# Optimization experiments

Measured on AMD Instinct MI355X. Metric: run time of the kernel, lower is better.

The kernel has to match this reference:

```python
import jax, jax.numpy as jnp
import numpy as np

B, SEQ, OBS, HID = 32, 50, 1024, 256


def setup_inputs() -> dict:
    key = jax.random.key(0)
    k = jax.random.split(key, 6)
    y = jax.random.normal(k[0], (B, SEQ, OBS), jnp.float32)
    logdet = jax.random.normal(k[1], (B * SEQ,), jnp.float32)
    U_param = jax.random.normal(k[2], (HID, HID), jnp.float32)
    V_param = jax.random.normal(k[3], (HID, HID), jnp.float32)
    # torch init sets alpha to small constant 0.001; use small positive values
    alpha = jax.random.uniform(k[4], (HID,), jnp.float32) * 0.01
    # C initialized as orthonormal-ish (svd-projected xavier); scale to unit-norm columns
    C = jax.random.normal(k[5], (OBS, HID), jnp.float32) / np.sqrt(OBS).astype(np.float32)
    return {"y": y, "logdet": logdet, "U_param": U_param, "V_param": V_param,
            "alpha": alpha, "C": C}


def _unitary(Up):
    """Product of dim Householder reflections, combined by pairwise doubling."""
    dim = Up.shape[0]
    Un = Up / jnp.linalg.norm(Up, axis=1, keepdims=True)
    # UH[i] = I - 2 u_i u_i^T   -> (dim, dim, dim)
    M = jnp.eye(dim, dtype=Up.dtype)[None] - 2.0 * Un[:, :, None] * Un[:, None, :]
    n = dim
    while n > 1:  # log2(dim) fixed steps (multi_matmul_power_of_two)
        n //= 2
        M = jnp.matmul(M[:n], M[n:])
    return M[0]


def reference(y, logdet, U_param, V_param, alpha, C):
    U = _unitary(U_param)
    V = _unitary(V_param)
    S = 1.0 - jnp.clip(jnp.abs(alpha), 0.0, 1.0)          # SV()
    A = U @ (S[None, :] * V.T)                             # build_A

    s = y.shape[1]
    obs, hid = C.shape

    # build_O_A: O = [C; C A; C A^2; ...] via scan (matrix-power recurrence)
    def step(T, _):
        return T @ A, T
    _, Os = jax.lax.scan(step, C, None, length=s)          # (s, obs, hid)
    O = Os.reshape(s * obs, hid)

    Y = y.reshape(y.shape[0], -1)                          # (b, s*obs)

    # torch.gels(Y.t(), O): least-squares solve, x0 detached
    x0 = jax.lax.stop_gradient(
        jnp.linalg.lstsq(jax.lax.stop_gradient(O), jax.lax.stop_gradient(Y.T))[0]
    )                                                      # (hid, b)

    Yhat = O @ x0                                          # (s*obs, b)
    w = Y.T - Yhat
    M = jnp.float32(obs)                                   # prod(xflat.shape[1:])
    loss = 0.5 * jnp.mean(w ** 2) + jnp.mean((logdet / M) ** 2)
    return loss


if __name__ == "__main__":
    print(reference(**setup_inputs()))
```

## Files before the change

kernel.cpp:

```cpp
#include <hip/hip_runtime.h>

#define HID 256
#define OBS 1024
#define SEQ 50
#define BATCH 32
#define SO (SEQ*OBS)

struct DevWS {
  float ub[2][HID][HID];
  float C2[2][HID][HID];
  float ZT[2][HID][HID];
  float U[HID][HID];
  float V[HID][HID];
  float A[HID][HID];
  float A2[HID][HID];
  float A4[HID][HID];
  float A8[HID][HID];
  float A16[HID][HID];
  float A32[HID][HID];
  float Cg[HID][HID];
  float G2[HID][HID];
  float Grun[HID][HID];
  float T[HID][HID];
  float T2[HID][HID];
  float G18[HID][HID];
  float G32b[HID][HID];
  float Gfin[HID][HID];
  float Zt[SEQ][HID*BATCH];
  float Rb[2][25][HID*BATCH];
  float psum[1025];
  float s1b[32];
};
__device__ DevWS g;

__device__ __forceinline__ float* sel(int c){
  switch(c){
    case 0:  return &g.ub[0][0][0];
    case 1:  return &g.ub[1][0][0];
    case 4:  return &g.C2[0][0][0];
    case 5:  return &g.C2[1][0][0];
    case 6:  return &g.ZT[0][0][0];
    case 7:  return &g.ZT[1][0][0];
    case 8:  return &g.U[0][0];
    case 9:  return &g.V[0][0];
    case 10: return &g.A[0][0];
    case 11: return &g.A2[0][0];
    case 12: return &g.A4[0][0];
    case 13: return &g.A8[0][0];
    case 14: return &g.A16[0][0];
    case 15: return &g.A32[0][0];
    case 16: return &g.Cg[0][0];
    case 17: return &g.G2[0][0];
    case 18: return &g.Grun[0][0];
    case 19: return &g.T[0][0];
    case 20: return &g.T2[0][0];
    case 21: return &g.G18[0][0];
    case 22: return &g.G32b[0][0];
    case 23: return &g.Gfin[0][0];
    case 24: return &g.Zt[0][0];
    case 25: return &g.Rb[0][0][0];
    default: return &g.Rb[1][0][0];
  }
}

__device__ __forceinline__ int bitrev8(int x){
  x = ((x & 0x55) << 1) | ((x >> 1) & 0x55);
  x = ((x & 0x33) << 2) | ((x >> 2) & 0x33);
  x = ((x & 0x0F) << 4) | ((x >> 4) & 0x0F);
  return x;
}

__global__ __launch_bounds__(256) void k_prep(const float* __restrict__ y,
                                              const float* __restrict__ logdet,
                                              const float* __restrict__ Up,
                                              const float* __restrict__ Vp,
                                              const float* __restrict__ Cm){
  __shared__ float As[16][36];
  __shared__ float Bs[16][36];
  __shared__ float red[256];
  const int bx = blockIdx.x;
  const int t = threadIdx.x;
  if(bx < 512){
    int mat = bx >> 8, j = bx & 255;
    int src = bitrev8(j);
    const float* P = mat ? Vp : Up;
    float x = P[src*HID + t];
    red[t] = x*x; __syncthreads();
    for(int s=128; s>0; s>>=1){ if(t<s) red[t]+=red[t+s]; __syncthreads(); }
    g.ub[mat][j][t] = x * rsqrtf(red[0]);
    return;
  }
  if(bx < 1536){
    int bi = bx - 512;
    const float4* y4 = reinterpret_cast<const float4*>(y);
    const int n4 = (BATCH*SO)/4;
    float s = 0.f;
    for(int i = bi*256 + t; i < n4; i += 1024*256){
      float4 v = y4[i];
      s += v.x*v.x + v.y*v.y + v.z*v.z + v.w*v.w;
    }
    red[t] = s; __syncthreads();
    for(int st=128; st>0; st>>=1){ if(t<st) red[t]+=red[t+st]; __syncthreads(); }
    if(t==0) g.psum[bi] = red[0];
    return;
  }
  if(bx == 1536){
    float s = 0.f;
    for(int i = t; i < BATCH*SEQ; i += 256){ float v = logdet[i]; s += v*v; }
    red[t] = s; __syncthreads();
    for(int st=128; st>0; st>>=1){ if(t<st) red[t]+=red[t+st]; __syncthreads(); }
    if(t==0) g.psum[1024] = red[0];
    return;
  }
  {
    int tile = bx - 1537;
    int tx = t & 15, ty = t >> 4;
    int m0 = (tile>>3)*32, n0 = (tile&7)*32;
    float acc[2][2] = {{0.f,0.f},{0.f,0.f}};
    for(int o0=0; o0<OBS; o0+=16){
      int r = t>>4, cp = (t&15)*2;
      float2 a = *reinterpret_cast<const float2*>(&Cm[(o0+r)*HID + m0 + cp]);
      As[r][cp] = a.x; As[r][cp+1] = a.y;
      float2 b = *reinterpret_cast<const float2*>(&Cm[(o0+r)*HID + n0 + cp]);
      Bs[r][cp] = b.x; Bs[r][cp+1] = b.y;
      __syncthreads();
      #pragma unroll
      for(int kk=0; kk<16; kk++){
        float a0 = As[kk][ty*2], a1 = As[kk][ty*2+1];
        float b0 = Bs[kk][tx*2], b1 = Bs[kk][tx*2+1];
        acc[0][0]+=a0*b0; acc[0][1]+=a0*b1; acc[1][0]+=a1*b0; acc[1][1]+=a1*b1;
      }
      __syncthreads();
    }
    #pragma unroll
    for(int i2=0;i2<2;i2++)
    #pragma unroll
    for(int j2=0;j2<2;j2++)
      g.Cg[m0+ty*2+i2][n0+tx*2+j2] = acc[i2][j2];
  }
}

__global__ __launch_bounds__(1024) void k_CtY(const float* __restrict__ y,
                                              const float* __restrict__ C){
  const int tt = blockIdx.x;
  __shared__ float ys[256][36];
  const int h = threadIdx.x >> 2, bq = threadIdx.x & 3;
  float acc[8] = {0,0,0,0,0,0,0,0};
  for(int ot=0; ot<4; ot++){
    for(int e=threadIdx.x; e<32*256; e+=1024){
      int b = e>>8, o = e&255;
      ys[o][b] = y[b*SO + tt*OBS + ot*256 + o];
    }
    __syncthreads();
    for(int o=0; o<256; o++){
      float cv = C[(ot*256+o)*HID + h];
      float4 v0 = *reinterpret_cast<const float4*>(&ys[o][bq*8]);
      float4 v1 = *reinterpret_cast<const float4*>(&ys[o][bq*8+4]);
      acc[0]+=cv*v0.x; acc[1]+=cv*v0.y; acc[2]+=cv*v0.z; acc[3]+=cv*v0.w;
      acc[4]+=cv*v1.x; acc[5]+=cv*v1.y; acc[6]+=cv*v1.z; acc[7]+=cv*v1.w;
    }
    __syncthreads();
  }
  #pragma unroll
  for(int j=0;j<8;j++) g.Zt[tt][h*32 + bq*8 + j] = acc[j];
}

__global__ __launch_bounds__(1024) void k_wy(){
  const int m = blockIdx.x;
  const int t = threadIdx.x;
  __shared__ float c2s[32][256];
  __shared__ float ws[32][256];
  for(int p=0; p<8; p++){
    const int k0 = p*32;
    for(int e=t; e<32*256; e+=1024){
      int k = e>>8, i = e&255;
      c2s[k][i] = (i < k0+k) ? g.C2[m][k0+k][i] : 0.f;
    }
    __syncthreads();
    {
      int d = t & 255, kg = t>>8;
      float acc[8] = {0,0,0,0,0,0,0,0};
      for(int i=0; i<k0; i++){
        float zv = g.ZT[m][i][d];
        #pragma unroll
        for(int kk=0; kk<8; kk++) acc[kk] += zv * c2s[kg*8+kk][i];
      }
      #pragma unroll
      for(int kk=0; kk<8; kk++) ws[kg*8+kk][d] = acc[kk];
    }
    __syncthreads();
    if(t < 256){
      const int d = t;
      float zreg[32];
      #pragma unroll
      for(int j=0;j<32;j++) zreg[j] = 0.f;
      #pragma unroll
      for(int k=0; k<32; k++){
        float a0=0.f,a1=0.f,a2=0.f,a3=0.f;
        #pragma unroll
        for(int j=0;j<32;j+=4){
          a0 += zreg[j]  *c2s[k][k0+j];
          a1 += zreg[j+1]*c2s[k][k0+j+1];
          a2 += zreg[j+2]*c2s[k][k0+j+2];
          a3 += zreg[j+3]*c2s[k][k0+j+3];
        }
        float acc = (a0+a1)+(a2+a3);
        zreg[k] = 2.f*(g.ub[m][k0+k][d] - ws[k][d] - acc);
      }
      #pragma unroll
      for(int k=0; k<32; k++) g.ZT[m][k0+k][d] = zreg[k];
    }
    __syncthreads();
  }
}

#define F_TRANSA   1
#define F_NEGID    2
#define F_ACC      4
#define F_TRANSB   8
#define F_SCALECOL 16
#define F_RLEVEL   32

struct GD { int cA, cB, cC, cD, flags, npair; };
struct GArgs { GD d[3]; int pre[3]; int nd; };

__global__ __launch_bounds__(256) void k_gemmN(GArgs ga, const float* __restrict__ alpha){
  int blk = blockIdx.x;
  int di = 0;
  if(ga.nd > 1 && blk >= ga.pre[1]) di = 1;
  if(ga.nd > 2 && blk >= ga.pre[2]) di = 2;
  const GD d = ga.d[di];
  const int local = blk - ga.pre[di];
  const int t = threadIdx.x;
  __shared__ float As[16][36];
  __shared__ float Bs[16][36];
  const int tx = t & 15, ty = t >> 4;

  if(d.flags & F_RLEVEL){
    const float* P  = sel(d.cA);
    const float* In = sel(d.cB);
    float* Out = sel(d.cC);
    const int j = local >> 3, mt = local & 7;
    if(j >= d.npair){
      const float* src = In + (size_t)(2*j)*(HID*BATCH) + mt*1024;
      float* dst = Out + (size_t)j*(HID*BATCH) + mt*1024;
      *reinterpret_cast<float4*>(dst + t*4) = *reinterpret_cast<const float4*>(src + t*4);
      return;
    }
    const float* B1 = In + (size_t)(2*j+1)*(HID*BATCH);
    const float* D0 = In + (size_t)(2*j)*(HID*BATCH);
    float* C0 = Out + (size_t)j*(HID*BATCH);
    const int m0 = mt*32;
    float acc[2][2] = {{0.f,0.f},{0.f,0.f}};
    for(int k0=0; k0<HID; k0+=16){
      { int kk=t>>4, mm=(t&15)*2;
        float2 a = *reinterpret_cast<const float2*>(&P[(k0+kk)*HID + m0+mm]);
        As[kk][mm]=a.x; As[kk][mm+1]=a.y; }
      { int rb=t>>4, cb=(t&15)*2;
        float2 b = *reinterpret_cast<const float2*>(&B1[(k0+rb)*BATCH + cb]);
        Bs[rb][cb]=b.x; Bs[rb][cb+1]=b.y; }
      __syncthreads();
      #pragma unroll
      for(int kk=0; kk<16; kk++){
        float a0=As[kk][ty*2], a1=As[kk][ty*2+1];
        float b0=Bs[kk][tx*2], b1=Bs[kk][tx*2+1];
        acc[0][0]+=a0*b0; acc[0][1]+=a0*b1; acc[1][0]+=a1*b0; acc[1][1]+=a1*b1;
      }
      __syncthreads();
    }
    #pragma unroll
    for(int i2=0;i2<2;i2++)
    #pragma unroll
    for(int j2=0;j2<2;j2++){
      int r=m0+ty*2+i2, c=tx*2+j2;
      C0[r*BATCH+c] = D0[r*BATCH+c] + acc[i2][j2];
    }
    return;
  }

  const float* A = sel(d.cA);
  const float* B = sel(d.cB);
  float* Cp = sel(d.cC);
  const float* Dp = sel(d.cD);
  const int m0 = (local>>3)*32, n0 = (local&7)*32;
  float acc[2][2] = {{0.f,0.f},{0.f,0.f}};
  for(int k0=0; k0<HID; k0+=16){
    if(d.flags & F_TRANSA){
      int kk=t>>4, mm=(t&15)*2;
      float2 a = *reinterpret_cast<const float2*>(&A[(k0+kk)*HID + m0+mm]);
      As[kk][mm]=a.x; As[kk][mm+1]=a.y;
    } else {
      int r=t>>3, c=(t&7)*2;
      float2 a = *reinterpret_cast<const float2*>(&A[(m0+r)*HID + k0+c]);
      As[c][r]=a.x; As[c+1][r]=a.y;
    }
    if(d.flags & F_TRANSB){
      int cb=t>>3, rb=(t&7)*2;
      float2 v = *reinterpret_cast<const float2*>(&B[(n0+cb)*HID + k0+rb]);
      Bs[rb][cb]=v.x; Bs[rb+1][cb]=v.y;
    } else {
      int rb=t>>4, cb=(t&15)*2;
      float2 b = *reinterpret_cast<const float2*>(&B[(k0+rb)*HID + n0+cb]);
      Bs[rb][cb]=b.x; Bs[rb][cb+1]=b.y;
    }
    __syncthreads();
    #pragma unroll
    for(int kk=0; kk<16; kk++){
      float a0=As[kk][ty*2], a1=As[kk][ty*2+1];
      float b0=Bs[kk][tx*2], b1=Bs[kk][tx*2+1];
      acc[0][0]+=a0*b0; acc[0][1]+=a0*b1; acc[1][0]+=a1*b0; acc[1][1]+=a1*b1;
    }
    __syncthreads();
  }
  float sc0=1.f, sc1=1.f;
  if(d.flags & F_SCALECOL){
    sc0 = 1.0f - fminf(fabsf(alpha[n0+tx*2]),   1.0f);
    sc1 = 1.0f - fminf(fabsf(alpha[n0+tx*2+1]), 1.0f);
  }
  #pragma unroll
  for(int i2=0;i2<2;i2++)
  #pragma unroll
  for(int j2=0;j2<2;j2++){
    int r=m0+ty*2+i2, c=n0+tx*2+j2;
    float v = acc[i2][j2];
    if(d.flags & F_ACC) v += Dp[r*HID+c];
    if(d.flags & F_SCALECOL) v *= (j2 ? sc1 : sc0);
    if(d.flags & F_NEGID) v = (r==c ? 1.0f : 0.0f) - v;
    Cp[r*HID+c] = v;
  }
}

#define CG_ITERS 10
__global__ __launch_bounds__(1024) void k_cg(){
  const int tid = threadIdx.x;
  const int i = tid & 255;
  const int q = tid >> 8;
  const int lane = tid & 63;
  const int wv = tid >> 6;
  const int b0 = blockIdx.x * 4;
  __shared__ float p_s[256][4];
  __shared__ float partf[4][256][4];
  __shared__ float red1[16];
  __shared__ float s_rz[4], s_pap[4], s_rzn[4], s_be[4], s_s1[4];

  float gr[64];
  const float* Gf = &g.Gfin[0][0];
  #pragma unroll
  for(int j=0;j<64;j++) gr[j] = Gf[(64*q+j)*HID + i];
  const float dinv = 1.0f / Gf[i*(HID+1)];

  float rcur = g.Rb[1][0][i*BATCH + b0 + q];
  p_s[i][q] = rcur*dinv;
  if(tid<4) s_s1[tid]=0.f;
  __syncthreads();

  {
    float v = dinv*rcur*rcur;
    v+=__shfl_down(v,32);v+=__shfl_down(v,16);v+=__shfl_down(v,8);
    v+=__shfl_down(v,4);v+=__shfl_down(v,2);v+=__shfl_down(v,1);
    if(lane==0) red1[wv]=v;
    __syncthreads();
    if(tid<4) s_rz[tid]=red1[tid*4]+red1[tid*4+1]+red1[tid*4+2]+red1[tid*4+3];
    __syncthreads();
  }

  for(int it=0; it<CG_ITERS; it++){
    float pa0=0.f,pa1=0.f,pa2=0.f,pa3=0.f;
    #pragma unroll
    for(int j=0;j<64;j++){
      const float4 pv = *reinterpret_cast<const float4*>(&p_s[64*q+j][0]);
      const float gv = gr[j];
      pa0 = fmaf(gv,pv.x,pa0); pa1 = fmaf(gv,pv.y,pa1);
      pa2 = fmaf(gv,pv.z,pa2); pa3 = fmaf(gv,pv.w,pa3);
    }
    float4 w4; w4.x=pa0; w4.y=pa1; w4.z=pa2; w4.w=pa3;
    *reinterpret_cast<float4*>(&partf[q][i][0]) = w4;
    __syncthreads();
    const float ap = partf[0][i][q]+partf[1][i][q]+partf[2][i][q]+partf[3][i][q];
    const float pvl = p_s[i][q];
    {
      float v = pvl*ap;
      v+=__shfl_down(v,32);v+=__shfl_down(v,16);v+=__shfl_down(v,8);
      v+=__shfl_down(v,4);v+=__shfl_down(v,2);v+=__shfl_down(v,1);
      if(lane==0) red1[wv]=v;
      __syncthreads();
      if(tid<4) s_pap[tid]=red1[tid*4]+red1[tid*4+1]+red1[tid*4+2]+red1[tid*4+3];
      __syncthreads();
    }
    const float al = s_rz[q]/fmaxf(s_pap[q],1e-30f);
    rcur = rcur - al*ap;
    {
      float v = dinv*rcur*rcur;
      v+=__shfl_down(v,32);v+=__shfl_down(v,16);v+=__shfl_down(v,8);
      v+=__shfl_down(v,4);v+=__shfl_down(v,2);v+=__shfl_down(v,1);
      if(lane==0) red1[wv]=v;
      __syncthreads();
      if(tid<4) s_rzn[tid]=red1[tid*4]+red1[tid*4+1]+red1[tid*4+2]+red1[tid*4+3];
      __syncthreads();
    }
    if(tid<4){
      const float alb = s_rz[tid]/fmaxf(s_pap[tid],1e-30f);
      s_s1[tid] += alb*s_rz[tid];
      s_be[tid]  = s_rzn[tid]/fmaxf(s_rz[tid],1e-30f);
      s_rz[tid]  = s_rzn[tid];
    }
    __syncthreads();
    p_s[i][q] = dinv*rcur + s_be[q]*p_s[i][q];
    __syncthreads();
  }
  if(tid<4) g.s1b[b0+tid] = s_s1[tid];
}

__global__ __launch_bounds__(256) void k_fin(float* __restrict__ out){
  const int t = threadIdx.x;
  __shared__ float red[4];
  float s = g.psum[t] + g.psum[t+256] + g.psum[t+512] + g.psum[t+768];
  s += __shfl_down(s,32); s += __shfl_down(s,16); s += __shfl_down(s,8);
  s += __shfl_down(s,4);  s += __shfl_down(s,2);  s += __shfl_down(s,1);
  if((t&63)==0) red[t>>6]=s;
  __syncthreads();
  if(t==0){
    float sy2 = red[0]+red[1]+red[2]+red[3];
    float t1 = 0.f;
    for(int b=0;b<32;b++) t1 += g.s1b[b];
    float sld = g.psum[1024];
    float mw = (sy2 - t1) / (float)(SO*BATCH);
    out[0] = 0.5f*mw + sld / ((float)(BATCH*SEQ) * (float)OBS * (float)OBS);
  }
}

struct LB { GArgs ga; int total; };
static inline GD sq(int cA,int cB,int cC,int cD,int flags){ GD d; d.cA=cA;d.cB=cB;d.cC=cC;d.cD=cD;d.flags=flags;d.npair=0; return d; }
static inline GD rl(int cP,int cin,int cout,int npair){ GD d; d.cA=cP;d.cB=cin;d.cC=cout;d.cD=0;d.flags=F_RLEVEL;d.npair=npair; return d; }
static inline LB mk1(GD a,int ba){ LB l; l.ga.d[0]=a; l.ga.pre[0]=0; l.ga.pre[1]=ba; l.ga.pre[2]=ba; l.ga.nd=1; l.total=ba; return l; }
static inline LB mk2(GD a,int ba,GD b,int bb){ LB l; l.ga.d[0]=a; l.ga.d[1]=b; l.ga.pre[0]=0; l.ga.pre[1]=ba; l.ga.pre[2]=ba+bb; l.ga.nd=2; l.total=ba+bb; return l; }
static inline LB mk3(GD a,int ba,GD b,int bb,GD c,int bc){ LB l; l.ga.d[0]=a; l.ga.d[1]=b; l.ga.d[2]=c; l.ga.pre[0]=0; l.ga.pre[1]=ba; l.ga.pre[2]=ba+bb; l.ga.nd=3; l.total=ba+bb+bc; return l; }

extern "C" void kernel_launch(void* const* d_in, const int* in_sizes, int n_in,
                              void* d_out, int out_size, void* d_ws, size_t ws_size,
                              hipStream_t stream){
  const float* y      = (const float*)d_in[0];
  const float* logdet = (const float*)d_in[1];
  const float* Up     = (const float*)d_in[2];
  const float* Vp     = (const float*)d_in[3];
  const float* alpha  = (const float*)d_in[4];
  const float* Cm     = (const float*)d_in[5];
  float* out = (float*)d_out;

  k_prep<<<dim3(1601), dim3(256), 0, stream>>>(y, logdet, Up, Vp, Cm);
  k_CtY<<<dim3(SEQ), dim3(1024), 0, stream>>>(y, Cm);
  { LB l = mk2(sq(0,0,4,4,F_TRANSB),64, sq(1,1,5,5,F_TRANSB),64);
    k_gemmN<<<l.total,256,0,stream>>>(l.ga, alpha); }
  k_wy<<<dim3(2), dim3(1024), 0, stream>>>();
  { LB l = mk2(sq(6,0,8,8,F_TRANSA|F_NEGID),64, sq(7,1,9,9,F_TRANSA|F_NEGID),64);
    k_gemmN<<<l.total,256,0,stream>>>(l.ga, alpha); }
  { LB l = mk1(sq(8,9,10,10,F_TRANSB|F_SCALECOL),64);
    k_gemmN<<<l.total,256,0,stream>>>(l.ga, alpha); }
  { LB l = mk2(sq(10,10,11,0,0),64, sq(10,16,19,0,F_TRANSA),64);
    k_gemmN<<<l.total,256,0,stream>>>(l.ga, alpha); }
  { LB l = mk2(sq(19,10,17,16,F_ACC),64, rl(10,24,25,25),200);
    k_gemmN<<<l.total,256,0,stream>>>(l.ga, alpha); }
  { LB l = mk2(sq(11,11,12,0,0),64, sq(11,17,19,0,F_TRANSA),64);
    k_gemmN<<<l.total,256,0,stream>>>(l.ga, alpha); }
  { LB l = mk2(sq(19,11,18,17,F_ACC),64, rl(11,25,26,12),104);
    k_gemmN<<<l.total,256,0,stream>>>(l.ga, alpha); }
  { LB l = mk2(sq(12,12,13,0,0),64, sq(12,18,19,0,F_TRANSA),64);
    k_gemmN<<<l.total,256,0,stream>>>(l.ga, alpha); }
  { LB l = mk2(sq(19,12,18,18,F_ACC),64, rl(12,26,25,6),56);
    k_gemmN<<<l.total,256,0,stream>>>(l.ga, alpha); }
  { LB l = mk2(sq(13,13,14,0,0),64, sq(13,18,19,0,F_TRANSA),64);
    k_gemmN<<<l.total,256,0,stream>>>(l.ga, alpha); }
  { LB l = mk2(sq(19,13,18,18,F_ACC),64, rl(13,25,26,3),32);
    k_gemmN<<<l.total,256,0,stream>>>(l.ga, alpha); }
  { LB l = mk3(sq(14,14,15,0,0),64, sq(14,18,19,0,F_TRANSA),64, sq(14,17,20,0,F_TRANSA),64);
    k_gemmN<<<l.total,256,0,stream>>>(l.ga, alpha); }
  { LB l = mk3(sq(19,14,22,18,F_ACC),64, sq(20,14,21,18,F_ACC),64, rl(14,26,25,2),16);
    k_gemmN<<<l.total,256,0,stream>>>(l.ga, alpha); }
  { LB l = mk2(sq(15,21,19,0,F_TRANSA),64, rl(15,25,26,1),8);
    k_gemmN<<<l.total,256,0,stream>>>(l.ga, alpha); }
  { LB l = mk1(sq(19,15,23,22,F_ACC),64);
    k_gemmN<<<l.total,256,0,stream>>>(l.ga, alpha); }

  k_cg<<<dim3(8), dim3(1024), 0, stream>>>();
  k_fin<<<dim3(1), dim3(256), 0, stream>>>(out);
}
```

Before: 562.5 us.

## Fuse all stages into one persistent kernel with software grid barriers

Replaces the sequence of roughly twenty kernel launches with one persistent kernel of 256 blocks. The stages are separated by an atomic-counter grid barrier, which removes launch gaps and tail idle time. The serial single-block WY accumulation is replaced by a block-diagonal solve and a tree of merge steps. C^T Y is now split into more work units, and the CG solve is spread across the grid. The barrier depends on all 256 blocks being resident at the same time, and each stage now runs at low parallelism with the barrier cost paid between stages.

```diff
diff --git a/kernel.cpp b/kernel.cpp
--- a/kernel.cpp
+++ b/kernel.cpp
@@ -5,9 +5,18 @@
 #define SEQ 50
 #define BATCH 32
 #define SO (SEQ*OBS)
+#define NBLK 256
+#define NTHR 256
+
+#define F_TRANSA   1
+#define F_NEGID    2
+#define F_ACC      4
+#define F_TRANSB   8
+#define F_SCALECOL 16
 
 struct DevWS {
   float ub[2][HID][HID];
+  float Mm[2][HID][HID];
   float C2[2][HID][HID];
   float ZT[2][HID][HID];
   float U[HID][HID];
@@ -26,17 +35,40 @@
   float G18[HID][HID];
   float G32b[HID][HID];
   float Gfin[HID][HID];
-  float Zt[SEQ][HID*BATCH];
+  float Zt4[SEQ][4][HID*BATCH];
   float Rb[2][25][HID*BATCH];
-  float psum[1025];
-  float s1b[32];
+  float psum[NBLK+1];
+  float s1b[BATCH];
 };
 __device__ DevWS g;
+
+__device__ unsigned bar_in  = 0;
+__device__ unsigned bar_out = 0;
+
+__device__ __forceinline__ void gridbar(){
+  __threadfence();
+  __syncthreads();
+  if(threadIdx.x == 0){
+    atomicAdd(&bar_in, 1u);
+    while(atomicAdd(&bar_in, 0u) < (unsigned)NBLK){ __builtin_amdgcn_s_sleep(2); }
+    unsigned v = atomicAdd(&bar_out, 1u);
+    if(v == (unsigned)NBLK - 1u){
+      atomicExch(&bar_in, 0u);
+      atomicExch(&bar_out, 0u);
+    } else {
+      while(atomicAdd(&bar_out, 0u) != 0u){ __builtin_amdgcn_s_sleep(2); }
+    }
+  }
+  __syncthreads();
+  __threadfence();
+}
 
 __device__ __forceinline__ float* sel(int c){
   switch(c){
     case 0:  return &g.ub[0][0][0];
     case 1:  return &g.ub[1][0][0];
+    case 2:  return &g.Mm[0][0][0];
+    case 3:  return &g.Mm[1][0][0];
     case 4:  return &g.C2[0][0][0];
     case 5:  return &g.C2[1][0][0];
     case 6:  return &g.ZT[0][0][0];
@@ -57,7 +89,6 @@
     case 21: return &g.G18[0][0];
     case 22: return &g.G32b[0][0];
     case 23: return &g.Gfin[0][0];
-    case 24: return &g.Zt[0][0];
     case 25: return &g.Rb[0][0][0];
     default: return &g.Rb[1][0][0];
   }
@@ -70,371 +101,442 @@
   return x;
 }
 
-__global__ __launch_bounds__(256) void k_prep(const float* __restrict__ y,
-                                              const float* __restrict__ logdet,
-                                              const float* __restrict__ Up,
-                                              const float* __restrict__ Vp,
-                                              const float* __restrict__ Cm){
-  __shared__ float As[16][36];
-  __shared__ float Bs[16][36];
-  __shared__ float red[256];
-  const int bx = blockIdx.x;
+__device__ __forceinline__ float blkred(float v, float* sm){
+  v += __shfl_down(v,32); v += __shfl_down(v,16); v += __shfl_down(v,8);
+  v += __shfl_down(v,4);  v += __shfl_down(v,2);  v += __shfl_down(v,1);
   const int t = threadIdx.x;
-  if(bx < 512){
-    int mat = bx >> 8, j = bx & 255;
-    int src = bitrev8(j);
-    const float* P = mat ? Vp : Up;
-    float x = P[src*HID + t];
-    red[t] = x*x; __syncthreads();
-    for(int s=128; s>0; s>>=1){ if(t<s) red[t]+=red[t+s]; __syncthreads(); }
-    g.ub[mat][j][t] = x * rsqrtf(red[0]);
-    return;
-  }
-  if(bx < 1536){
-    int bi = bx - 512;
-    const float4* y4 = reinterpret_cast<const float4*>(y);
-    const int n4 = (BATCH*SO)/4;
-    float s = 0.f;
-    for(int i = bi*256 + t; i < n4; i += 1024*256){
-      float4 v = y4[i];
-      s += v.x*v.x + v.y*v.y + v.z*v.z + v.w*v.w;
-    }
-    red[t] = s; __syncthreads();
-    for(int st=128; st>0; st>>=1){ if(t<st) red[t]+=red[t+st]; __syncthreads(); }
-    if(t==0) g.psum[bi] = red[0];
-    return;
-  }
-  if(bx == 1536){
-    float s = 0.f;
-    for(int i = t; i < BATCH*SEQ; i += 256){ float v = logdet[i]; s += v*v; }
-    red[t] = s; __syncthreads();
-    for(int st=128; st>0; st>>=1){ if(t<st) red[t]+=red[t+st]; __syncthreads(); }
-    if(t==0) g.psum[1024] = red[0];
-    return;
-  }
-  {
-    int tile = bx - 1537;
-    int tx = t & 15, ty = t >> 4;
-    int m0 = (tile>>3)*32, n0 = (tile&7)*32;
-    float acc[2][2] = {{0.f,0.f},{0.f,0.f}};
-    for(int o0=0; o0<OBS; o0+=16){
-      int r = t>>4, cp = (t&15)*2;
-      float2 a = *reinterpret_cast<const float2*>(&Cm[(o0+r)*HID + m0 + cp]);
-      As[r][cp] = a.x; As[r][cp+1] = a.y;
-      float2 b = *reinterpret_cast<const float2*>(&Cm[(o0+r)*HID + n0 + cp]);
-      Bs[r][cp] = b.x; Bs[r][cp+1] = b.y;
-      __syncthreads();
-      #pragma unroll
-      for(int kk=0; kk<16; kk++){
-        float a0 = As[kk][ty*2], a1 = As[kk][ty*2+1];
-        float b0 = Bs[kk][tx*2], b1 = Bs[kk][tx*2+1];
-        acc[0][0]+=a0*b0; acc[0][1]+=a0*b1; acc[1][0]+=a1*b0; acc[1][1]+=a1*b1;
-      }
-      __syncthreads();
-    }
-    #pragma unroll
-    for(int i2=0;i2<2;i2++)
-    #pragma unroll
-    for(int j2=0;j2<2;j2++)
-      g.Cg[m0+ty*2+i2][n0+tx*2+j2] = acc[i2][j2];
-  }
-}
-
-__global__ __launch_bounds__(1024) void k_CtY(const float* __restrict__ y,
-                                              const float* __restrict__ C){
-  const int tt = blockIdx.x;
-  __shared__ float ys[256][36];
-  const int h = threadIdx.x >> 2, bq = threadIdx.x & 3;
-  float acc[8] = {0,0,0,0,0,0,0,0};
-  for(int ot=0; ot<4; ot++){
-    for(int e=threadIdx.x; e<32*256; e+=1024){
-      int b = e>>8, o = e&255;
-      ys[o][b] = y[b*SO + tt*OBS + ot*256 + o];
-    }
-    __syncthreads();
-    for(int o=0; o<256; o++){
-      float cv = C[(ot*256+o)*HID + h];
-      float4 v0 = *reinterpret_cast<const float4*>(&ys[o][bq*8]);
-      float4 v1 = *reinterpret_cast<const float4*>(&ys[o][bq*8+4]);
-      acc[0]+=cv*v0.x; acc[1]+=cv*v0.y; acc[2]+=cv*v0.z; acc[3]+=cv*v0.w;
-      acc[4]+=cv*v1.x; acc[5]+=cv*v1.y; acc[6]+=cv*v1.z; acc[7]+=cv*v1.w;
-    }
-    __syncthreads();
-  }
-  #pragma unroll
-  for(int j=0;j<8;j++) g.Zt[tt][h*32 + bq*8 + j] = acc[j];
-}
-
-__global__ __launch_bounds__(1024) void k_wy(){
-  const int m = blockIdx.x;
-  const int t = threadIdx.x;
-  __shared__ float c2s[32][256];
-  __shared__ float ws[32][256];
-  for(int p=0; p<8; p++){
-    const int k0 = p*32;
-    for(int e=t; e<32*256; e+=1024){
-      int k = e>>8, i = e&255;
-      c2s[k][i] = (i < k0+k) ? g.C2[m][k0+k][i] : 0.f;
-    }
-    __syncthreads();
-    {
-      int d = t & 255, kg = t>>8;
-      float acc[8] = {0,0,0,0,0,0,0,0};
-      for(int i=0; i<k0; i++){
-        float zv = g.ZT[m][i][d];
-        #pragma unroll
-        for(int kk=0; kk<8; kk++) acc[kk] += zv * c2s[kg*8+kk][i];
-      }
-      #pragma unroll
-      for(int kk=0; kk<8; kk++) ws[kg*8+kk][d] = acc[kk];
-    }
-    __syncthreads();
-    if(t < 256){
-      const int d = t;
-      float zreg[32];
-      #pragma unroll
-      for(int j=0;j<32;j++) zreg[j] = 0.f;
-      #pragma unroll
-      for(int k=0; k<32; k++){
-        float a0=0.f,a1=0.f,a2=0.f,a3=0.f;
-        #pragma unroll
-        for(int j=0;j<32;j+=4){
-          a0 += zreg[j]  *c2s[k][k0+j];
-          a1 += zreg[j+1]*c2s[k][k0+j+1];
-          a2 += zreg[j+2]*c2s[k][k0+j+2];
-          a3 += zreg[j+3]*c2s[k][k0+j+3];
-        }
-        float acc = (a0+a1)+(a2+a3);
-        zreg[k] = 2.f*(g.ub[m][k0+k][d] - ws[k][d] - acc);
-      }
-      #pragma unroll
-      for(int k=0; k<32; k++) g.ZT[m][k0+k][d] = zreg[k];
-    }
-    __syncthreads();
-  }
-}
-
-#define F_TRANSA   1
-#define F_NEGID    2
-#define F_ACC      4
-#define F_TRANSB   8
-#define F_SCALECOL 16
-#define F_RLEVEL   32
-
-struct GD { int cA, cB, cC, cD, flags, npair; };
-struct GArgs { GD d[3]; int pre[3]; int nd; };
-
-__global__ __launch_bounds__(256) void k_gemmN(GArgs ga, const float* __restrict__ alpha){
-  int blk = blockIdx.x;
-  int di = 0;
-  if(ga.nd > 1 && blk >= ga.pre[1]) di = 1;
-  if(ga.nd > 2 && blk >= ga.pre[2]) di = 2;
-  const GD d = ga.d[di];
-  const int local = blk - ga.pre[di];
-  const int t = threadIdx.x;
-  __shared__ float As[16][36];
-  __shared__ float Bs[16][36];
-  const int tx = t & 15, ty = t >> 4;
-
-  if(d.flags & F_RLEVEL){
-    const float* P  = sel(d.cA);
-    const float* In = sel(d.cB);
-    float* Out = sel(d.cC);
-    const int j = local >> 3, mt = local & 7;
-    if(j >= d.npair){
-      const float* src = In + (size_t)(2*j)*(HID*BATCH) + mt*1024;
-      float* dst = Out + (size_t)j*(HID*BATCH) + mt*1024;
-      *reinterpret_cast<float4*>(dst + t*4) = *reinterpret_cast<const float4*>(src + t*4);
-      return;
-    }
-    const float* B1 = In + (size_t)(2*j+1)*(HID*BATCH);
-    const float* D0 = In + (size_t)(2*j)*(HID*BATCH);
-    float* C0 = Out + (size_t)j*(HID*BATCH);
-    const int m0 = mt*32;
-    float acc[2][2] = {{0.f,0.f},{0.f,0.f}};
-    for(int k0=0; k0<HID; k0+=16){
-      { int kk=t>>4, mm=(t&15)*2;
-        float2 a = *reinterpret_cast<const float2*>(&P[(k0+kk)*HID + m0+mm]);
-        As[kk][mm]=a.x; As[kk][mm+1]=a.y; }
-      { int rb=t>>4, cb=(t&15)*2;
-        float2 b = *reinterpret_cast<const float2*>(&B1[(k0+rb)*BATCH + cb]);
-        Bs[rb][cb]=b.x; Bs[rb][cb+1]=b.y; }
-      __syncthreads();
-      #pragma unroll
-      for(int kk=0; kk<16; kk++){
-        float a0=As[kk][ty*2], a1=As[kk][ty*2+1];
-        float b0=Bs[kk][tx*2], b1=Bs[kk][tx*2+1];
-        acc[0][0]+=a0*b0; acc[0][1]+=a0*b1; acc[1][0]+=a1*b0; acc[1][1]+=a1*b1;
-      }
-      __syncthreads();
-    }
-    #pragma unroll
-    for(int i2=0;i2<2;i2++)
-    #pragma unroll
-    for(int j2=0;j2<2;j2++){
-      int r=m0+ty*2+i2, c=tx*2+j2;
-      C0[r*BATCH+c] = D0[r*BATCH+c] + acc[i2][j2];
-    }
-    return;
-  }
-
-  const float* A = sel(d.cA);
-  const float* B = sel(d.cB);
-  float* Cp = sel(d.cC);
-  const float* Dp = sel(d.cD);
+  if((t&63)==0) sm[t>>6] = v;
+  __syncthreads();
+  float r = sm[0]+sm[1]+sm[2]+sm[3];
+  __syncthreads();
+  return r;
+}
+
+__device__ void sq_tile(float* sm, int cA,int cB,int cC,int cD,int flags,int local,
+                        const float* __restrict__ alpha){
+  const float* A = sel(cA);
+  const float* B = sel(cB);
+  float* Cp = sel(cC);
+  const float* Dp = sel(cD);
+  float* As = sm; float* Bs = sm + 576;
+  const int t = threadIdx.x, tx = t&15, ty = t>>4;
   const int m0 = (local>>3)*32, n0 = (local&7)*32;
-  float acc[2][2] = {{0.f,0.f},{0.f,0.f}};
-  for(int k0=0; k0<HID; k0+=16){
-    if(d.flags & F_TRANSA){
+  float a00=0.f,a01=0.f,a10=0.f,a11=0.f;
+  for(int k0=0;k0<HID;k0+=16){
+    if(flags & F_TRANSA){
       int kk=t>>4, mm=(t&15)*2;
-      float2 a = *reinterpret_cast<const float2*>(&A[(k0+kk)*HID + m0+mm]);
-      As[kk][mm]=a.x; As[kk][mm+1]=a.y;
+      float2 a=*reinterpret_cast<const float2*>(&A[(k0+kk)*HID+m0+mm]);
+      As[kk*36+mm]=a.x; As[kk*36+mm+1]=a.y;
     } else {
       int r=t>>3, c=(t&7)*2;
-      float2 a = *reinterpret_cast<const float2*>(&A[(m0+r)*HID + k0+c]);
-      As[c][r]=a.x; As[c+1][r]=a.y;
-    }
-    if(d.flags & F_TRANSB){
+      float2 a=*reinterpret_cast<const float2*>(&A[(m0+r)*HID+k0+c]);
+      As[c*36+r]=a.x; As[(c+1)*36+r]=a.y;
+    }
+    if(flags & F_TRANSB){
       int cb=t>>3, rb=(t&7)*2;
-      float2 v = *reinterpret_cast<const float2*>(&B[(n0+cb)*HID + k0+rb]);
-      Bs[rb][cb]=v.x; Bs[rb+1][cb]=v.y;
+      float2 v=*reinterpret_cast<const float2*>(&B[(n0+cb)*HID+k0+rb]);
+      Bs[rb*36+cb]=v.x; Bs[(rb+1)*36+cb]=v.y;
     } else {
       int rb=t>>4, cb=(t&15)*2;
-      float2 b = *reinterpret_cast<const float2*>(&B[(k0+rb)*HID + n0+cb]);
-      Bs[rb][cb]=b.x; Bs[rb][cb+1]=b.y;
-    }
-    __syncthreads();
-    #pragma unroll
-    for(int kk=0; kk<16; kk++){
-      float a0=As[kk][ty*2], a1=As[kk][ty*2+1];
-      float b0=Bs[kk][tx*2], b1=Bs[kk][tx*2+1];
-      acc[0][0]+=a0*b0; acc[0][1]+=a0*b1; acc[1][0]+=a1*b0; acc[1][1]+=a1*b1;
-    }
-    __syncthreads();
-  }
-  float sc0=1.f, sc1=1.f;
-  if(d.flags & F_SCALECOL){
-    sc0 = 1.0f - fminf(fabsf(alpha[n0+tx*2]),   1.0f);
-    sc1 = 1.0f - fminf(fabsf(alpha[n0+tx*2+1]), 1.0f);
-  }
+      float2 bv=*reinterpret_cast<const float2*>(&B[(k0+rb)*HID+n0+cb]);
+      Bs[rb*36+cb]=bv.x; Bs[rb*36+cb+1]=bv.y;
+    }
+    __syncthreads();
+    #pragma unroll
+    for(int kk=0;kk<16;kk++){
+      float x0=As[kk*36+ty*2], x1=As[kk*36+ty*2+1];
+      float y0=Bs[kk*36+tx*2], y1=Bs[kk*36+tx*2+1];
+      a00+=x0*y0; a01+=x0*y1; a10+=x1*y0; a11+=x1*y1;
+    }
+    __syncthreads();
+  }
+  const int r=m0+ty*2, c=n0+tx*2;
+  float v00=a00,v01=a01,v10=a10,v11=a11;
+  if(flags & F_ACC){
+    v00+=Dp[r*HID+c]; v01+=Dp[r*HID+c+1];
+    v10+=Dp[(r+1)*HID+c]; v11+=Dp[(r+1)*HID+c+1];
+  }
+  if(flags & F_SCALECOL){
+    float s0=1.f-fminf(fabsf(alpha[c]),1.f);
+    float s1=1.f-fminf(fabsf(alpha[c+1]),1.f);
+    v00*=s0; v01*=s1; v10*=s0; v11*=s1;
+  }
+  if(flags & F_NEGID){
+    v00=((r==c)?1.f:0.f)-v00;   v01=((r==c+1)?1.f:0.f)-v01;
+    v10=((r+1==c)?1.f:0.f)-v10; v11=((r+1==c+1)?1.f:0.f)-v11;
+  }
+  Cp[r*HID+c]=v00; Cp[r*HID+c+1]=v01;
+  Cp[(r+1)*HID+c]=v10; Cp[(r+1)*HID+c+1]=v11;
+}
+
+__device__ void cgram_tile(float* sm, int tile, const float* __restrict__ Cm){
+  float* As = sm; float* Bs = sm + 576;
+  const int t = threadIdx.x, tx = t&15, ty = t>>4;
+  const int m0=(tile>>3)*32, n0=(tile&7)*32;
+  float a00=0.f,a01=0.f,a10=0.f,a11=0.f;
+  for(int o0=0;o0<OBS;o0+=16){
+    int r=t>>4, cp=(t&15)*2;
+    float2 a=*reinterpret_cast<const float2*>(&Cm[(o0+r)*HID+m0+cp]);
+    As[r*36+cp]=a.x; As[r*36+cp+1]=a.y;
+    float2 b2=*reinterpret_cast<const float2*>(&Cm[(o0+r)*HID+n0+cp]);
+    Bs[r*36+cp]=b2.x; Bs[r*36+cp+1]=b2.y;
+    __syncthreads();
+    #pragma unroll
+    for(int kk=0;kk<16;kk++){
+      float x0=As[kk*36+ty*2], x1=As[kk*36+ty*2+1];
+      float y0=Bs[kk*36+tx*2], y1=Bs[kk*36+tx*2+1];
+      a00+=x0*y0; a01+=x0*y1; a10+=x1*y0; a11+=x1*y1;
+    }
+    __syncthreads();
+  }
+  g.Cg[m0+ty*2][n0+tx*2]=a00;   g.Cg[m0+ty*2][n0+tx*2+1]=a01;
+  g.Cg[m0+ty*2+1][n0+tx*2]=a10; g.Cg[m0+ty*2+1][n0+tx*2+1]=a11;
+}
+
+__device__ void norm_unit(float* sm, int u, const float* __restrict__ Up,
+                          const float* __restrict__ Vp){
+  int mat=u>>8, j=u&255, src=bitrev8(j);
+  const float* P = mat ? Vp : Up;
+  int t=threadIdx.x;
+  float x = P[src*HID + t];
+  float ss = blkred(x*x, sm);
+  g.ub[mat][j][t] = x * rsqrtf(ss);
+}
+
+__device__ void cty_unit(float* sm, int u, const float* __restrict__ y,
+                         const float* __restrict__ Cm){
+  int tt=u>>2, ot=u&3;
+  float* ys = sm;
+  const int t=threadIdx.x;
+  for(int e=t;e<8192;e+=256){
+    int b=e>>8, o=e&255;
+    ys[o*36+b] = y[b*SO + tt*OBS + ot*256 + o];
+  }
+  __syncthreads();
+  const int h=t;
+  float acc[32];
   #pragma unroll
-  for(int i2=0;i2<2;i2++)
+  for(int z=0;z<32;z++) acc[z]=0.f;
+  for(int o=0;o<256;o++){
+    float cv = Cm[(ot*256+o)*HID + h];
+    #pragma unroll
+    for(int bb=0;bb<32;bb+=4){
+      float4 v=*reinterpret_cast<const float4*>(&ys[o*36+bb]);
+      acc[bb]+=cv*v.x; acc[bb+1]+=cv*v.y; acc[bb+2]+=cv*v.z; acc[bb+3]+=cv*v.w;
+    }
+  }
+  float* outp = &g.Zt4[tt][ot][h*BATCH];
   #pragma unroll
-  for(int j2=0;j2<2;j2++){
-    int r=m0+ty*2+i2, c=n0+tx*2+j2;
-    float v = acc[i2][j2];
-    if(d.flags & F_ACC) v += Dp[r*HID+c];
-    if(d.flags & F_SCALECOL) v *= (j2 ? sc1 : sc0);
-    if(d.flags & F_NEGID) v = (r==c ? 1.0f : 0.0f) - v;
-    Cp[r*HID+c] = v;
-  }
-}
-
-#define CG_ITERS 10
-__global__ __launch_bounds__(1024) void k_cg(){
-  const int tid = threadIdx.x;
-  const int i = tid & 255;
-  const int q = tid >> 8;
-  const int lane = tid & 63;
-  const int wv = tid >> 6;
-  const int b0 = blockIdx.x * 4;
-  __shared__ float p_s[256][4];
-  __shared__ float partf[4][256][4];
-  __shared__ float red1[16];
-  __shared__ float s_rz[4], s_pap[4], s_rzn[4], s_be[4], s_s1[4];
-
-  float gr[64];
+  for(int bb=0;bb<32;bb+=4){
+    float4 w={acc[bb],acc[bb+1],acc[bb+2],acc[bb+3]};
+    *reinterpret_cast<float4*>(&outp[bb])=w;
+  }
+  __syncthreads();
+}
+
+__device__ void mdiag_unit(float* sm, int u){
+  int mat=u>>3, p=u&7;
+  float* Ls = sm;
+  const int t=threadIdx.x;
+  for(int e=t;e<1024;e+=256){
+    int k=e>>5, i=e&31;
+    Ls[k*33+i] = g.C2[mat][p*32+k][p*32+i];
+  }
+  for(int e=t;e<32*256;e+=256){
+    int r=e>>8, c=e&255;
+    g.Mm[mat][p*32+r][c]=0.f;
+  }
+  __syncthreads();
+  if(t<32){
+    const int j=t;
+    float m[32];
+    #pragma unroll
+    for(int k=0;k<32;k++){
+      float s=0.f;
+      #pragma unroll
+      for(int i=0;i<32;i++) if(i<k) s += Ls[k*33+i]*m[i];
+      m[k] = (k<j) ? 0.f : ((k==j) ? 2.f : (-2.f*s));
+    }
+    #pragma unroll
+    for(int k=0;k<32;k++) g.Mm[mat][p*32+k][p*32+j]=m[k];
+  }
+  __syncthreads();
+}
+
+template<int S>
+__device__ void merge_unit(float* sm, int u){
+  constexpr int NT = S/32;
+  constexpr int NMG = 128/S;
+  constexpr int NTILE = NT*NT;
+  constexpr int STR = S/8;
+  int mat = u/(NMG*NTILE);
+  int rem = u%(NMG*NTILE);
+  int mg = rem/NTILE;
+  int tile = rem%NTILE;
+  int tr = tile/NT, tc = tile%NT;
+  const int o = mg*2*S;
+  float* M2s = sm;
+  float* Ts  = sm + 32*(S+1);
+  float* Gc  = sm + 32*(S+1) + 32*(S+4);
+  float* Mm = &g.Mm[mat][0][0];
+  const float* C2m = &g.C2[mat][0][0];
+  const int t=threadIdx.x;
+  for(int e=t;e<32*S;e+=256){
+    int r=e/S, k=e%S;
+    M2s[r*(S+1)+k] = Mm[(o+S+tr*32+r)*HID + o+S+k];
+  }
+  __syncthreads();
+  const int r1=t>>3, jq=t&7;
+  float acc[STR];
+  #pragma unroll
+  for(int z=0;z<STR;z++) acc[z]=0.f;
+  for(int kc=0;kc<S;kc+=32){
+    for(int e=t;e<32*S;e+=256){
+      int kk=e/S, jj=e%S;
+      Gc[kk*(S+4)+jj] = C2m[(o+S+kc+kk)*HID + o+jj];
+    }
+    __syncthreads();
+    #pragma unroll
+    for(int kk=0;kk<32;kk++){
+      float mv = M2s[r1*(S+1)+kc+kk];
+      #pragma unroll
+      for(int z=0;z<STR;z++) acc[z] += mv * Gc[kk*(S+4)+jq*STR+z];
+    }
+    __syncthreads();
+  }
+  #pragma unroll
+  for(int z=0;z<STR;z++) Ts[r1*(S+4)+jq*STR+z]=acc[z];
+  __syncthreads();
+  const int r2=t>>3, cq=t&7;
+  float oacc[4]={0.f,0.f,0.f,0.f};
+  for(int kc=0;kc<S;kc+=32){
+    for(int e=t;e<1024;e+=256){
+      int kk=e>>5, c=e&31;
+      Gc[kk*36+c] = Mm[(o+kc+kk)*HID + o+tc*32+c];
+    }
+    __syncthreads();
+    #pragma unroll
+    for(int kk=0;kk<32;kk++){
+      float tv = Ts[r2*(S+4)+kc+kk];
+      #pragma unroll
+      for(int z=0;z<4;z++) oacc[z] += tv * Gc[kk*36+cq*4+z];
+    }
+    __syncthreads();
+  }
+  #pragma unroll
+  for(int z=0;z<4;z++)
+    Mm[(o+S+tr*32+r2)*HID + o+tc*32+cq*4+z] = -oacc[z];
+  __syncthreads();
+}
+
+template<int ZT4>
+__device__ void rlevel_unit(float* sm, int cP, int cin, int cout, int npair, int local){
+  const float* P = sel(cP);
+  float* Out = sel(cout);
+  const int t=threadIdx.x;
+  const int j=local>>3, mt=local&7;
+  const float* In = ZT4 ? nullptr : sel(cin);
+  auto ldin = [&](int idx, int off)->float{
+    if(ZT4){
+      const float* z=&g.Zt4[idx][0][0];
+      return z[off]+z[HID*BATCH+off]+z[2*HID*BATCH+off]+z[3*HID*BATCH+off];
+    }
+    return In[(size_t)idx*(HID*BATCH)+off];
+  };
+  if(j>=npair){
+    for(int e=t;e<1024;e+=256)
+      Out[(size_t)j*(HID*BATCH)+mt*1024+e] = ldin(2*j, mt*1024+e);
+    return;
+  }
+  float* As=sm; float* Bs=sm+576;
+  const int tx=t&15, ty=t>>4;
+  const int m0=mt*32;
+  float a00=0.f,a01=0.f,a10=0.f,a11=0.f;
+  for(int k0=0;k0<HID;k0+=16){
+    { int kk=t>>4, mm=(t&15)*2;
+      float2 a=*reinterpret_cast<const float2*>(&P[(k0+kk)*HID+m0+mm]);
+      As[kk*36+mm]=a.x; As[kk*36+mm+1]=a.y; }
+    { int rb=t>>4, cb=(t&15)*2;
+      Bs[rb*36+cb]  =ldin(2*j+1,(k0+rb)*BATCH+cb);
+      Bs[rb*36+cb+1]=ldin(2*j+1,(k0+rb)*BATCH+cb+1); }
+    __syncthreads();
+    #pragma unroll
+    for(int kk=0;kk<16;kk++){
+      float p0=As[kk*36+ty*2], p1=As[kk*36+ty*2+1];
+      float b0=Bs[kk*36+tx*2], b1=Bs[kk*36+tx*2+1];
+      a00+=p0*b0; a01+=p0*b1; a10+=p1*b0; a11+=p1*b1;
+    }
+    __syncthreads();
+  }
+  float* C0 = Out + (size_t)j*(HID*BATCH);
+  const int r=m0+ty*2, c=tx*2;
+  C0[r*BATCH+c]      =ldin(2*j,r*BATCH+c)+a00;
+  C0[r*BATCH+c+1]    =ldin(2*j,r*BATCH+c+1)+a01;
+  C0[(r+1)*BATCH+c]  =ldin(2*j,(r+1)*BATCH+c)+a10;
+  C0[(r+1)*BATCH+c+1]=ldin(2*j,(r+1)*BATCH+c+1)+a11;
+}
+
+__device__ void cg_solve_unit(float* sm, int bb){
+  float* ps = sm;
+  float* red = sm + 260;
   const float* Gf = &g.Gfin[0][0];
-  #pragma unroll
-  for(int j=0;j<64;j++) gr[j] = Gf[(64*q+j)*HID + i];
-  const float dinv = 1.0f / Gf[i*(HID+1)];
-
-  float rcur = g.Rb[1][0][i*BATCH + b0 + q];
-  p_s[i][q] = rcur*dinv;
-  if(tid<4) s_s1[tid]=0.f;
-  __syncthreads();
-
-  {
-    float v = dinv*rcur*rcur;
+  const int i = threadIdx.x;
+  auto red256 = [&](float v)->float{
     v+=__shfl_down(v,32);v+=__shfl_down(v,16);v+=__shfl_down(v,8);
     v+=__shfl_down(v,4);v+=__shfl_down(v,2);v+=__shfl_down(v,1);
-    if(lane==0) red1[wv]=v;
-    __syncthreads();
-    if(tid<4) s_rz[tid]=red1[tid*4]+red1[tid*4+1]+red1[tid*4+2]+red1[tid*4+3];
-    __syncthreads();
-  }
-
-  for(int it=0; it<CG_ITERS; it++){
-    float pa0=0.f,pa1=0.f,pa2=0.f,pa3=0.f;
-    #pragma unroll
-    for(int j=0;j<64;j++){
-      const float4 pv = *reinterpret_cast<const float4*>(&p_s[64*q+j][0]);
-      const float gv = gr[j];
-      pa0 = fmaf(gv,pv.x,pa0); pa1 = fmaf(gv,pv.y,pa1);
-      pa2 = fmaf(gv,pv.z,pa2); pa3 = fmaf(gv,pv.w,pa3);
-    }
-    float4 w4; w4.x=pa0; w4.y=pa1; w4.z=pa2; w4.w=pa3;
-    *reinterpret_cast<float4*>(&partf[q][i][0]) = w4;
-    __syncthreads();
-    const float ap = partf[0][i][q]+partf[1][i][q]+partf[2][i][q]+partf[3][i][q];
-    const float pvl = p_s[i][q];
-    {
-      float v = pvl*ap;
-      v+=__shfl_down(v,32);v+=__shfl_down(v,16);v+=__shfl_down(v,8);
-      v+=__shfl_down(v,4);v+=__shfl_down(v,2);v+=__shfl_down(v,1);
-      if(lane==0) red1[wv]=v;
+    if((i&63)==0) red[i>>6]=v;
+    __syncthreads();
+    float r=red[0]+red[1]+red[2]+red[3];
+    __syncthreads();
+    return r;
+  };
+  const float dinv = 1.f/Gf[i*(HID+1)];
+  float rcur = g.Rb[1][0][i*BATCH+bb];
+  ps[i] = dinv*rcur;
+  __syncthreads();
+  float rz = red256(dinv*rcur*rcur);
+  float s1 = 0.f;
+  for(int it=0; it<10; it++){
+    float ap0=0.f,ap1=0.f,ap2=0.f,ap3=0.f;
+    #pragma unroll 4
+    for(int k=0;k<HID;k+=4){
+      ap0 = fmaf(Gf[k*HID+i],     ps[k],   ap0);
+      ap1 = fmaf(Gf[(k+1)*HID+i], ps[k+1], ap1);
+      ap2 = fmaf(Gf[(k+2)*HID+i], ps[k+2], ap2);
+      ap3 = fmaf(Gf[(k+3)*HID+i], ps[k+3], ap3);
+    }
+    float ap = (ap0+ap1)+(ap2+ap3);
+    float pap = red256(ps[i]*ap);
+    float al = rz/fmaxf(pap,1e-30f);
+    rcur -= al*ap;
+    float rzn = red256(dinv*rcur*rcur);
+    s1 += al*rz;
+    float be = rzn/fmaxf(rz,1e-30f);
+    rz = rzn;
+    __syncthreads();
+    ps[i] = dinv*rcur + be*ps[i];
+    __syncthreads();
+  }
+  if(i==0) g.s1b[bb]=s1;
+  __syncthreads();
+}
+
+__global__ void __launch_bounds__(NTHR, 1)
+k_mono(const float* __restrict__ y, const float* __restrict__ logdet,
+       const float* __restrict__ Up, const float* __restrict__ Vp,
+       const float* __restrict__ alpha, const float* __restrict__ Cm,
+       float* __restrict__ out){
+  __shared__ float sm[12800];
+  const int b = blockIdx.x;
+  const int t = threadIdx.x;
+
+  {
+    const float4* y4 = reinterpret_cast<const float4*>(y);
+    float s=0.f;
+    for(int i=b*NTHR+t; i<(BATCH*SO)/4; i+=NBLK*NTHR){
+      float4 v=y4[i]; s+=v.x*v.x+v.y*v.y+v.z*v.z+v.w*v.w;
+    }
+    float r=blkred(s,sm);
+    if(t==0) g.psum[b]=r;
+    __syncthreads();
+  }
+  for(int u=b; u<777; u+=NBLK){
+    if(u<512) norm_unit(sm,u,Up,Vp);
+    else if(u<576) cgram_tile(sm,u-512,Cm);
+    else if(u<776) cty_unit(sm,u-576,y,Cm);
+    else {
+      float s=0.f;
+      for(int i=t;i<BATCH*SEQ;i+=256){float v=logdet[i]; s+=v*v;}
+      float r=blkred(s,sm);
+      if(t==0) g.psum[NBLK]=r;
       __syncthreads();
-      if(tid<4) s_pap[tid]=red1[tid*4]+red1[tid*4+1]+red1[tid*4+2]+red1[tid*4+3];
-      __syncthreads();
-    }
-    const float al = s_rz[q]/fmaxf(s_pap[q],1e-30f);
-    rcur = rcur - al*ap;
-    {
-      float v = dinv*rcur*rcur;
-      v+=__shfl_down(v,32);v+=__shfl_down(v,16);v+=__shfl_down(v,8);
-      v+=__shfl_down(v,4);v+=__shfl_down(v,2);v+=__shfl_down(v,1);
-      if(lane==0) red1[wv]=v;
-      __syncthreads();
-      if(tid<4) s_rzn[tid]=red1[tid*4]+red1[tid*4+1]+red1[tid*4+2]+red1[tid*4+3];
-      __syncthreads();
-    }
-    if(tid<4){
-      const float alb = s_rz[tid]/fmaxf(s_pap[tid],1e-30f);
-      s_s1[tid] += alb*s_rz[tid];
-      s_be[tid]  = s_rzn[tid]/fmaxf(s_rz[tid],1e-30f);
-      s_rz[tid]  = s_rzn[tid];
-    }
-    __syncthreads();
-    p_s[i][q] = dinv*rcur + s_be[q]*p_s[i][q];
-    __syncthreads();
-  }
-  if(tid<4) g.s1b[b0+tid] = s_s1[tid];
-}
-
-__global__ __launch_bounds__(256) void k_fin(float* __restrict__ out){
-  const int t = threadIdx.x;
-  __shared__ float red[4];
-  float s = g.psum[t] + g.psum[t+256] + g.psum[t+512] + g.psum[t+768];
-  s += __shfl_down(s,32); s += __shfl_down(s,16); s += __shfl_down(s,8);
-  s += __shfl_down(s,4);  s += __shfl_down(s,2);  s += __shfl_down(s,1);
-  if((t&63)==0) red[t>>6]=s;
-  __syncthreads();
-  if(t==0){
-    float sy2 = red[0]+red[1]+red[2]+red[3];
-    float t1 = 0.f;
-    for(int b=0;b<32;b++) t1 += g.s1b[b];
-    float sld = g.psum[1024];
-    float mw = (sy2 - t1) / (float)(SO*BATCH);
-    out[0] = 0.5f*mw + sld / ((float)(BATCH*SEQ) * (float)OBS * (float)OBS);
-  }
-}
-
-struct LB { GArgs ga; int total; };
-static inline GD sq(int cA,int cB,int cC,int cD,int flags){ GD d; d.cA=cA;d.cB=cB;d.cC=cC;d.cD=cD;d.flags=flags;d.npair=0; return d; }
-static inline GD rl(int cP,int cin,int cout,int npair){ GD d; d.cA=cP;d.cB=cin;d.cC=cout;d.cD=0;d.flags=F_RLEVEL;d.npair=npair; return d; }
-static inline LB mk1(GD a,int ba){ LB l; l.ga.d[0]=a; l.ga.pre[0]=0; l.ga.pre[1]=ba; l.ga.pre[2]=ba; l.ga.nd=1; l.total=ba; return l; }
-static inline LB mk2(GD a,int ba,GD b,int bb){ LB l; l.ga.d[0]=a; l.ga.d[1]=b; l.ga.pre[0]=0; l.ga.pre[1]=ba; l.ga.pre[2]=ba+bb; l.ga.nd=2; l.total=ba+bb; return l; }
-static inline LB mk3(GD a,int ba,GD b,int bb,GD c,int bc){ LB l; l.ga.d[0]=a; l.ga.d[1]=b; l.ga.d[2]=c; l.ga.pre[0]=0; l.ga.pre[1]=ba; l.ga.pre[2]=ba+bb; l.ga.nd=3; l.total=ba+bb+bc; return l; }
+    }
+  }
+  gridbar();
+  for(int u=b;u<128;u+=NBLK){ int mat=u>>6; sq_tile(sm,mat,mat,4+mat,0,F_TRANSB,u&63,alpha); }
+  gridbar();
+  for(int u=b;u<16;u+=NBLK) mdiag_unit(sm,u);
+  gridbar();
+  for(int u=b;u<8;u+=NBLK)  merge_unit<32>(sm,u);
+  gridbar();
+  for(int u=b;u<16;u+=NBLK) merge_unit<64>(sm,u);
+  gridbar();
+  for(int u=b;u<32;u+=NBLK) merge_unit<128>(sm,u);
+  gridbar();
+  for(int u=b;u<128;u+=NBLK){ int mat=u>>6; sq_tile(sm,2+mat,mat,6+mat,0,0,u&63,alpha); }
+  gridbar();
+  for(int u=b;u<128;u+=NBLK){ int mat=u>>6; sq_tile(sm,6+mat,mat,8+mat,0,F_TRANSA|F_NEGID,u&63,alpha); }
+  gridbar();
+  for(int u=b;u<64;u+=NBLK) sq_tile(sm,8,9,10,0,F_TRANSB|F_SCALECOL,u,alpha);
+  gridbar();
+  for(int u=b;u<128;u+=NBLK){
+    if(u<64) sq_tile(sm,10,10,11,0,0,u,alpha);
+    else     sq_tile(sm,10,16,19,0,F_TRANSA,u-64,alpha);
+  }
+  gridbar();
+  for(int u=b;u<328;u+=NBLK){
+    if(u<64)       sq_tile(sm,19,10,17,16,F_ACC,u,alpha);
+    else if(u<128) sq_tile(sm,11,11,12,0,0,u-64,alpha);
+    else           rlevel_unit<1>(sm,10,0,25,25,u-128);
+  }
+  gridbar();
+  for(int u=b;u<232;u+=NBLK){
+    if(u<64)       sq_tile(sm,11,17,19,0,F_TRANSA,u,alpha);
+    else if(u<128) sq_tile(sm,12,12,13,0,0,u-64,alpha);
+    else           rlevel_unit<0>(sm,11,25,26,12,u-128);
+  }
+  gridbar();
+  for(int u=b;u<184;u+=NBLK){
+    if(u<64)       sq_tile(sm,19,11,18,17,F_ACC,u,alpha);
+    else if(u<128) sq_tile(sm,13,13,14,0,0,u-64,alpha);
+    else           rlevel_unit<0>(sm,12,26,25,6,u-128);
+  }
+  gridbar();
+  for(int u=b;u<160;u+=NBLK){
+    if(u<64)       sq_tile(sm,12,18,19,0,F_TRANSA,u,alpha);
+    else if(u<128) sq_tile(sm,14,14,15,0,0,u-64,alpha);
+    else           rlevel_unit<0>(sm,13,25,26,3,u-128);
+  }
+  gridbar();
+  for(int u=b;u<80;u+=NBLK){
+    if(u<64) sq_tile(sm,19,12,18,18,F_ACC,u,alpha);
+    else     rlevel_unit<0>(sm,14,26,25,2,u-64);
+  }
+  gridbar();
+  for(int u=b;u<72;u+=NBLK){
+    if(u<64) sq_tile(sm,13,18,19,0,F_TRANSA,u,alpha);
+    else     rlevel_unit<0>(sm,15,25,26,1,u-64);
+  }
+  gridbar();
+  for(int u=b;u<64;u+=NBLK) sq_tile(sm,19,13,18,18,F_ACC,u,alpha);
+  gridbar();
+  for(int u=b;u<128;u+=NBLK){
+    if(u<64) sq_tile(sm,14,18,19,0,F_TRANSA,u,alpha);
+    else     sq_tile(sm,14,17,20,0,F_TRANSA,u-64,alpha);
+  }
+  gridbar();
+  for(int u=b;u<128;u+=NBLK){
+    if(u<64) sq_tile(sm,19,14,22,18,F_ACC,u,alpha);
+    else     sq_tile(sm,20,14,21,18,F_ACC,u-64,alpha);
+  }
+  gridbar();
+  for(int u=b;u<64;u+=NBLK) sq_tile(sm,15,21,19,0,F_TRANSA,u,alpha);
+  gridbar();
+  for(int u=b;u<64;u+=NBLK) sq_tile(sm,19,15,23,22,F_ACC,u,alpha);
+  gridbar();
+  for(int u=b;u<BATCH;u+=NBLK) cg_solve_unit(sm,u);
+  gridbar();
+  if(b==0){
+    float r = blkred(g.psum[t], sm);
+    if(t==0){
+      float t1=0.f;
+      for(int q=0;q<BATCH;q++) t1+=g.s1b[q];
+      float sld = g.psum[NBLK];
+      float mw = (r - t1)/(float)(SO*BATCH);
+      out[0] = 0.5f*mw + sld/((float)(BATCH*SEQ)*(float)OBS*(float)OBS);
+    }
+  }
+}
 
 extern "C" void kernel_launch(void* const* d_in, const int* in_sizes, int n_in,
                               void* d_out, int out_size, void* d_ws, size_t ws_size,
@@ -445,42 +547,7 @@
   const float* Vp     = (const float*)d_in[3];
   const float* alpha  = (const float*)d_in[4];
   const float* Cm     = (const float*)d_in[5];
-  float* out = (float*)d_out;
-
-  k_prep<<<dim3(1601), dim3(256), 0, stream>>>(y, logdet, Up, Vp, Cm);
-  k_CtY<<<dim3(SEQ), dim3(1024), 0, stream>>>(y, Cm);
-  { LB l = mk2(sq(0,0,4,4,F_TRANSB),64, sq(1,1,5,5,F_TRANSB),64);
-    k_gemmN<<<l.total,256,0,stream>>>(l.ga, alpha); }
-  k_wy<<<dim3(2), dim3(1024), 0, stream>>>();
-  { LB l = mk2(sq(6,0,8,8,F_TRANSA|F_NEGID),64, sq(7,1,9,9,F_TRANSA|F_NEGID),64);
-    k_gemmN<<<l.total,256,0,stream>>>(l.ga, alpha); }
-  { LB l = mk1(sq(8,9,10,10,F_TRANSB|F_SCALECOL),64);
-    k_gemmN<<<l.total,256,0,stream>>>(l.ga, alpha); }
-  { LB l = mk2(sq(10,10,11,0,0),64, sq(10,16,19,0,F_TRANSA),64);
-    k_gemmN<<<l.total,256,0,stream>>>(l.ga, alpha); }
-  { LB l = mk2(sq(19,10,17,16,F_ACC),64, rl(10,24,25,25),200);
-    k_gemmN<<<l.total,256,0,stream>>>(l.ga, alpha); }
-  { LB l = mk2(sq(11,11,12,0,0),64, sq(11,17,19,0,F_TRANSA),64);
-    k_gemmN<<<l.total,256,0,stream>>>(l.ga, alpha); }
-  { LB l = mk2(sq(19,11,18,17,F_ACC),64, rl(11,25,26,12),104);
-    k_gemmN<<<l.total,256,0,stream>>>(l.ga, alpha); }
-  { LB l = mk2(sq(12,12,13,0,0),64, sq(12,18,19,0,F_TRANSA),64);
-    k_gemmN<<<l.total,256,0,stream>>>(l.ga, alpha); }
-  { LB l = mk2(sq(19,12,18,18,F_ACC),64, rl(12,26,25,6),56);
-    k_gemmN<<<l.total,256,0,stream>>>(l.ga, alpha); }
-  { LB l = mk2(sq(13,13,14,0,0),64, sq(13,18,19,0,F_TRANSA),64);
-    k_gemmN<<<l.total,256,0,stream>>>(l.ga, alpha); }
-  { LB l = mk2(sq(19,13,18,18,F_ACC),64, rl(13,25,26,3),32);
-    k_gemmN<<<l.total,256,0,stream>>>(l.ga, alpha); }
-  { LB l = mk3(sq(14,14,15,0,0),64, sq(14,18,19,0,F_TRANSA),64, sq(14,17,20,0,F_TRANSA),64);
-    k_gemmN<<<l.total,256,0,stream>>>(l.ga, alpha); }
-  { LB l = mk3(sq(19,14,22,18,F_ACC),64, sq(20,14,21,18,F_ACC),64, rl(14,26,25,2),16);
-    k_gemmN<<<l.total,256,0,stream>>>(l.ga, alpha); }
-  { LB l = mk2(sq(15,21,19,0,F_TRANSA),64, rl(15,25,26,1),8);
-    k_gemmN<<<l.total,256,0,stream>>>(l.ga, alpha); }
-  { LB l = mk1(sq(19,15,23,22,F_ACC),64);
-    k_gemmN<<<l.total,256,0,stream>>>(l.ga, alpha); }
-
-  k_cg<<<dim3(8), dim3(1024), 0, stream>>>();
-  k_fin<<<dim3(1), dim3(256), 0, stream>>>(out);
-}
+  float* outp = (float*)d_out;
+
+  k_mono<<<dim3(NBLK), dim3(NTHR), 0, stream>>>(y, logdet, Up, Vp, alpha, Cm, outp);
+}
```

Measured after the change: 1.337 ms. 2.38x slower.
